# Performance work log

Hardware: AMD Instinct MI355X
Metric: run time of the kernel (lower is better)

Reference implementation:

```python
import jax, jax.numpy as jnp
import numpy as np

# SamplesLoss('sinkhorn', p=2, blur=0.05, scaling=0.5, diameter=2.0, debias=True, backend='tensorized')
P = 2
BLUR = 0.05
SCALING = 0.5
DIAMETER = 2.0


def epsilon_schedule(p, diameter, blur, scaling):
    # geomloss epsilon annealing: diameter^p -> blur^p, geometric in eps
    eps_list = (
        [diameter ** p]
        + [np.exp(e) for e in np.arange(p * np.log(diameter), p * np.log(blur), p * np.log(scaling))]
        + [blur ** p]
    )
    return [float(e) for e in eps_list]


def softmin(eps, C, h):
    # soft C-transform: f_i = -eps * log sum_j exp(h_j - C_ij/eps)
    # C: (B,N,M), h: (B,M) -> (B,N)
    return -eps * jax.scipy.special.logsumexp(h[:, None, :] - C / eps, axis=2)


def sq_cost(x, y):
    # SqDist(x,y)/2 : (B,N,D),(B,M,D) -> (B,N,M)
    x2 = jnp.sum(x * x, axis=-1)[:, :, None]
    y2 = jnp.sum(y * y, axis=-1)[:, None, :]
    return (x2 + y2 - 2.0 * jnp.einsum('bnd,bmd->bnm', x, y)) * 0.5


def setup_inputs() -> dict:
    key = jax.random.key(0)
    k1, k2 = jax.random.split(key)
    x = jax.random.uniform(k1, (8, 2048, 3), dtype=jnp.float32)
    y = jax.random.uniform(k2, (8, 2048, 3), dtype=jnp.float32)
    return {"x": x, "y": y}


def reference(x, y):
    B, N, _ = x.shape
    M = y.shape[1]
    # uniform weights (SamplesLoss default when only point clouds are given)
    a_log = jnp.full((B, N), -float(np.log(N)), dtype=x.dtype)
    b_log = jnp.full((B, M), -float(np.log(M)), dtype=y.dtype)

    C_xy = sq_cost(x, y)                 # (B,N,M)
    C_yx = jnp.swapaxes(C_xy, 1, 2)      # (B,M,N)
    C_xx = sq_cost(x, x)                 # (B,N,N) debias term
    C_yy = sq_cost(y, y)                 # (B,M,M) debias term

    eps_list = epsilon_schedule(P, DIAMETER, BLUR, SCALING)

    # initialization at the coarsest temperature (balanced OT: damping = 1)
    eps0 = eps_list[0]
    f_aa = softmin(eps0, C_xx, a_log)
    g_bb = softmin(eps0, C_yy, b_log)
    g_ab = softmin(eps0, C_yx, a_log)
    f_ba = softmin(eps0, C_xy, b_log)

    # symmetric Sinkhorn loop with epsilon scaling (no grad tracked in torch here)
    for eps in eps_list:
        ft_ba = softmin(eps, C_xy, b_log + g_ab / eps)
        gt_ab = softmin(eps, C_yx, a_log + f_ba / eps)
        f_ba = 0.5 * (f_ba + ft_ba)
        g_ab = 0.5 * (g_ab + gt_ab)
        ft_aa = softmin(eps, C_xx, a_log + f_aa / eps)
        gt_bb = softmin(eps, C_yy, b_log + g_bb / eps)
        f_aa = 0.5 * (f_aa + ft_aa)
        g_bb = 0.5 * (g_bb + gt_bb)

    # last extrapolation step, with detached dual potentials (torch .detach())
    eps = eps_list[-1]
    sg = jax.lax.stop_gradient
    f_ba, g_ab = (
        softmin(eps, C_xy, b_log + sg(g_ab) / eps),
        softmin(eps, C_yx, a_log + sg(f_ba) / eps),
    )
    f_aa = softmin(eps, C_xx, a_log + sg(f_aa) / eps)
    g_bb = softmin(eps, C_yy, b_log + sg(g_bb) / eps)

    # debiased Sinkhorn divergence, batch mode -> (B,)
    a = jnp.exp(a_log)
    b = jnp.exp(b_log)
    return jnp.sum(a * (f_ba - f_aa), axis=-1) + jnp.sum(b * (g_ab - g_bb), axis=-1)
```

## Files before the change

### kernel.cpp

```cpp
#include <hip/hip_runtime.h>
#include <math.h>

#define BATCH 8
#define NPTS 2048
#define THREADS 256
#define HALF_COLS 1024
#define NTILES_H 64
#define FRAGS 2
#define ROWS_PER_WAVE 32
#define ROWS_PER_BLOCK 128
#define LOG_M 7.62559580411076

typedef __attribute__((ext_vector_type(8))) __bf16 bf16x8;
typedef __attribute__((ext_vector_type(4))) float f32x4;

union FragU { unsigned short u[8]; uint4 v; };

__device__ __forceinline__ unsigned short f2bf(float f) {
    union { float f; unsigned u; } x; x.f = f;
    unsigned r = x.u + 0x7FFFu + ((x.u >> 16) & 1u);
    return (unsigned short)(r >> 16);
}
__device__ __forceinline__ float bf2f(unsigned short b) {
    union { unsigned u; float f; } x; x.u = ((unsigned)b) << 16;
    return x.f;
}

__global__ __launch_bounds__(THREADS) void softmin_pass(
    const float* __restrict__ x, const float* __restrict__ y,
    const float* __restrict__ potSrc, float* __restrict__ potDst,
    float sigma, float k2, float inv_k2, float rowc0, int avg)
{
    __shared__ uint4 BF[NTILES_H][32];
    __shared__ uint4 AF[4][FRAGS][32];
    __shared__ float NM[ROWS_PER_BLOCK];

    const int type  = blockIdx.z;
    const int batch = blockIdx.y;

    const float* rowP;
    const float* colP;
    int hslot, oslot;
    if (type == 0)      { rowP = x; colP = y; hslot = 1; oslot = 0; }
    else if (type == 1) { rowP = y; colP = x; hslot = 0; oslot = 1; }
    else if (type == 2) { rowP = x; colP = x; hslot = 2; oslot = 2; }
    else                { rowP = y; colP = y; hslot = 3; oslot = 3; }

    rowP += batch * NPTS * 3;
    colP += batch * NPTS * 3;
    const float* hP   = potSrc + (hslot * BATCH + batch) * NPTS;
    const float* oldP = potSrc + (oslot * BATCH + batch) * NPTS;
    float*       outP = potDst + (oslot * BATCH + batch) * NPTS;

    {
        const int t = threadIdx.x;
        const int w = t >> 6, fr = (t >> 5) & 1, idx = t & 31;
        const int row = blockIdx.x * ROWS_PER_BLOCK + w * ROWS_PER_WAVE
                      + fr * 16 + (idx & 15);
        float x0 = rowP[3 * row + 0], x1 = rowP[3 * row + 1], x2 = rowP[3 * row + 2];
        float p0 = sigma * (x0 - 0.5f), p1 = sigma * (x1 - 0.5f), p2 = sigma * (x2 - 0.5f);
        unsigned short h0 = f2bf(p0); unsigned short l0 = f2bf(p0 - bf2f(h0));
        unsigned short h1 = f2bf(p1); unsigned short l1 = f2bf(p1 - bf2f(h1));
        unsigned short h2 = f2bf(p2); unsigned short l2 = f2bf(p2 - bf2f(h2));
        FragU f;
        if (idx < 16) {
            f.u[0] = h0; f.u[1] = h0; f.u[2] = l0; f.u[3] = l0;
            f.u[4] = h1; f.u[5] = h1; f.u[6] = l1; f.u[7] = l1;
        } else {
            f.u[0] = h2; f.u[1] = h2; f.u[2] = l2; f.u[3] = l2;
            f.u[4] = 0x3F80; f.u[5] = 0x3F80; f.u[6] = 0x3F80; f.u[7] = 0;
        }
        AF[w][fr][idx] = f.v;
    }

    if (threadIdx.x < ROWS_PER_BLOCK) {
        const int i = blockIdx.x * ROWS_PER_BLOCK + threadIdx.x;
        float x0 = rowP[3 * i + 0], x1 = rowP[3 * i + 1], x2 = rowP[3 * i + 2];
        float p0 = x0 - 0.5f, p1 = x1 - 0.5f, p2 = x2 - 0.5f;
        float rowconst = 0.5f * (p0 * p0 + p1 * p1 + p2 * p2) + rowc0;
        NM[threadIdx.x] = (oldP[i] - rowconst) * inv_k2;
    }

    const int lane = threadIdx.x & 63;
    const int wave = threadIdx.x >> 6;
    const int lidx = lane & 31;
    const int quad = lane >> 4;

    float s[FRAGS][4] = {{0,0,0,0},{0,0,0,0}};
    bf16x8 af0, af1;
    f32x4 nm0, nm1;

    for (int h = 0; h < 2; ++h) {
        if (h) __syncthreads();

        for (int jj = threadIdx.x; jj < HALF_COLS; jj += THREADS) {
            const int j = h * HALF_COLS + jj;
            float y0 = colP[3 * j + 0], y1 = colP[3 * j + 1], y2 = colP[3 * j + 2];
            float p0 = y0 - 0.5f, p1 = y1 - 0.5f, p2 = y2 - 0.5f;
            unsigned short h0 = f2bf(p0); unsigned short l0 = f2bf(p0 - bf2f(h0));
            unsigned short h1 = f2bf(p1); unsigned short l1 = f2bf(p1 - bf2f(h1));
            unsigned short h2 = f2bf(p2); unsigned short l2 = f2bf(p2 - bf2f(h2));
            float hhe = sigma * (hP[j] - 0.5f * (p0 * p0 + p1 * p1 + p2 * p2));
            unsigned short hA = f2bf(hhe); float r1 = hhe - bf2f(hA);
            unsigned short hB = f2bf(r1);  float r2 = r1 - bf2f(hB);
            unsigned short hC = f2bf(r2);
            FragU f0, f1;
            f0.u[0] = h0; f0.u[1] = l0; f0.u[2] = h0; f0.u[3] = l0;
            f0.u[4] = h1; f0.u[5] = l1; f0.u[6] = h1; f0.u[7] = l1;
            f1.u[0] = h2; f1.u[1] = l2; f1.u[2] = h2; f1.u[3] = l2;
            f1.u[4] = hA; f1.u[5] = hB; f1.u[6] = hC; f1.u[7] = 0;
            BF[jj >> 4][jj & 15]        = f0.v;
            BF[jj >> 4][16 + (jj & 15)] = f1.v;
        }
        __syncthreads();

        if (h == 0) {
            af0 = *(const bf16x8*)&AF[wave][0][lidx];
            af1 = *(const bf16x8*)&AF[wave][1][lidx];
            nm0 = *(const f32x4*)&NM[wave * ROWS_PER_WAVE + quad * 4];
            nm1 = *(const f32x4*)&NM[wave * ROWS_PER_WAVE + 16 + quad * 4];
        }

        #pragma unroll 4
        for (int t = 0; t < NTILES_H; ++t) {
            bf16x8 bf = *(const bf16x8*)&BF[t][lidx];
            f32x4 a0 = __builtin_amdgcn_mfma_f32_16x16x32_bf16(af0, bf, nm0, 0, 0, 0);
            f32x4 a1 = __builtin_amdgcn_mfma_f32_16x16x32_bf16(af1, bf, nm1, 0, 0, 0);
            #pragma unroll
            for (int r = 0; r < 4; ++r) {
                s[0][r] += __builtin_amdgcn_exp2f(a0[r]);
                s[1][r] += __builtin_amdgcn_exp2f(a1[r]);
            }
        }
    }

    #pragma unroll
    for (int off = 1; off <= 8; off <<= 1)
        #pragma unroll
        for (int f = 0; f < FRAGS; ++f)
            #pragma unroll
            for (int r = 0; r < 4; ++r)
                s[f][r] += __shfl_xor(s[f][r], off, 64);

    if ((lane & 15) == 0) {
        #pragma unroll
        for (int f = 0; f < FRAGS; ++f) {
            #pragma unroll
            for (int r = 0; r < 4; ++r) {
                const int i = blockIdx.x * ROWS_PER_BLOCK + wave * ROWS_PER_WAVE
                            + f * 16 + quad * 4 + r;
                float oldv = oldP[i];
                float res = oldv - k2 * __log2f(s[f][r]);
                outP[i] = avg ? 0.5f * (oldv + res) : res;
            }
        }
    }
}

__global__ void reduce_out(const float* __restrict__ pot, float* __restrict__ out)
{
    const int batch = blockIdx.x;
    const float* fba = pot + (0 * BATCH + batch) * NPTS;
    const float* gab = pot + (1 * BATCH + batch) * NPTS;
    const float* faa = pot + (2 * BATCH + batch) * NPTS;
    const float* gbb = pot + (3 * BATCH + batch) * NPTS;

    float s = 0.0f;
    for (int i = threadIdx.x; i < NPTS; i += blockDim.x)
        s += (fba[i] - faa[i]) + (gab[i] - gbb[i]);

    #pragma unroll
    for (int off = 32; off >= 1; off >>= 1)
        s += __shfl_xor(s, off, 64);

    __shared__ float red[THREADS / 64];
    const int lane = threadIdx.x & 63;
    const int wave = threadIdx.x >> 6;
    if (lane == 0) red[wave] = s;
    __syncthreads();
    if (threadIdx.x == 0) {
        float t = 0.0f;
        for (int w = 0; w < THREADS / 64; ++w) t += red[w];
        out[batch] = t * (1.0f / NPTS);
    }
}

extern "C" void kernel_launch(void* const* d_in, const int* in_sizes, int n_in,
                              void* d_out, int out_size, void* d_ws, size_t ws_size,
                              hipStream_t stream)
{
    const float* x = (const float*)d_in[0];
    const float* y = (const float*)d_in[1];
    float* out = (float*)d_out;

    const size_t potElems = (size_t)4 * BATCH * NPTS;
    float* P0 = (float*)d_ws;
    float* P1 = P0 + potElems;

    hipMemsetAsync(P0, 0, potElems * sizeof(float), stream);

    double epsl[16];
    int ne = 0;
    epsl[ne++] = 4.0;
    const double stop = 2.0 * log(0.05);
    const double step = 2.0 * log(0.5);
    for (double e = 2.0 * log(2.0); e > stop; e += step)
        epsl[ne++] = exp(e);
    epsl[ne++] = 0.05 * 0.05;

    float* src = P0;
    float* dst = P1;
    dim3 grid(NPTS / ROWS_PER_BLOCK, BATCH, 4);

    auto launch = [&](double eps, int avg) {
        float sigma  = (float)(M_LOG2E / (2.0 * eps));
        float k2     = (float)(eps * M_LN2);
        float inv_k2 = (float)(1.0 / (eps * M_LN2));
        float rowc0  = (float)(eps * LOG_M);
        softmin_pass<<<grid, THREADS, 0, stream>>>(
            x, y, src, dst, sigma, k2, inv_k2, rowc0, avg);
        float* t = src; src = dst; dst = t;
    };

    launch(epsl[0], 0);
    for (int k = 0; k < ne; ++k)
        launch(epsl[k], 1);
    launch(epsl[ne - 1], 0);

    reduce_out<<<dim3(BATCH), THREADS, 0, stream>>>(src, out);
}
```

Before: 284.6 us.

## Switch to 32x32x16 MFMA tiles with column-split waves and LDS row reduction

Replaces the 16x16x32 bf16 MFMA (two fragments per wave, 128 rows per block) with the 32x32x16 variant. Each pair of waves shares 32 rows and splits the column tiles, and partial row sums are merged through shared memory before the log step. Blocks shrink to 64 rows, doubling the grid, and sigma's scaling is adjusted to match the new operand packing. The intent is higher MFMA throughput per instruction and more blocks for occupancy, at the cost of an extra LDS reduction and barrier. Each MFMA now feeds 16 exp2 calls, so exp throughput probably remains the bottleneck.

```diff
diff --git a/kernel.cpp b/kernel.cpp
--- a/kernel.cpp
+++ b/kernel.cpp
@@ -5,14 +5,12 @@
 #define NPTS 2048
 #define THREADS 256
 #define HALF_COLS 1024
-#define NTILES_H 64
-#define FRAGS 2
-#define ROWS_PER_WAVE 32
-#define ROWS_PER_BLOCK 128
+#define TILES_H 32
+#define ROWS_PER_BLOCK 64
 #define LOG_M 7.62559580411076
 
-typedef __attribute__((ext_vector_type(8))) __bf16 bf16x8;
-typedef __attribute__((ext_vector_type(4))) float f32x4;
+typedef __attribute__((ext_vector_type(8)))  __bf16 bf16x8;
+typedef __attribute__((ext_vector_type(16))) float  f32x16;
 
 union FragU { unsigned short u[8]; uint4 v; };
 
@@ -31,9 +29,10 @@
     const float* __restrict__ potSrc, float* __restrict__ potDst,
     float sigma, float k2, float inv_k2, float rowc0, int avg)
 {
-    __shared__ uint4 BF[NTILES_H][32];
-    __shared__ uint4 AF[4][FRAGS][32];
+    __shared__ uint4 BF[TILES_H][64];
+    __shared__ uint4 AF[2][64];
     __shared__ float NM[ROWS_PER_BLOCK];
+    __shared__ float SRED[2][2][32];
 
     const int type  = blockIdx.z;
     const int batch = blockIdx.y;
@@ -52,43 +51,43 @@
     const float* oldP = potSrc + (oslot * BATCH + batch) * NPTS;
     float*       outP = potDst + (oslot * BATCH + batch) * NPTS;
 
-    {
-        const int t = threadIdx.x;
-        const int w = t >> 6, fr = (t >> 5) & 1, idx = t & 31;
-        const int row = blockIdx.x * ROWS_PER_BLOCK + w * ROWS_PER_WAVE
-                      + fr * 16 + (idx & 15);
+    if (threadIdx.x < 128) {
+        const int g = threadIdx.x >> 6, idx = threadIdx.x & 63;
+        const int row = blockIdx.x * ROWS_PER_BLOCK + g * 32 + (idx & 31);
         float x0 = rowP[3 * row + 0], x1 = rowP[3 * row + 1], x2 = rowP[3 * row + 2];
         float p0 = sigma * (x0 - 0.5f), p1 = sigma * (x1 - 0.5f), p2 = sigma * (x2 - 0.5f);
         unsigned short h0 = f2bf(p0); unsigned short l0 = f2bf(p0 - bf2f(h0));
         unsigned short h1 = f2bf(p1); unsigned short l1 = f2bf(p1 - bf2f(h1));
         unsigned short h2 = f2bf(p2); unsigned short l2 = f2bf(p2 - bf2f(h2));
         FragU f;
-        if (idx < 16) {
+        if (idx < 32) {
             f.u[0] = h0; f.u[1] = h0; f.u[2] = l0; f.u[3] = l0;
             f.u[4] = h1; f.u[5] = h1; f.u[6] = l1; f.u[7] = l1;
         } else {
             f.u[0] = h2; f.u[1] = h2; f.u[2] = l2; f.u[3] = l2;
             f.u[4] = 0x3F80; f.u[5] = 0x3F80; f.u[6] = 0x3F80; f.u[7] = 0;
         }
-        AF[w][fr][idx] = f.v;
-    }
-
-    if (threadIdx.x < ROWS_PER_BLOCK) {
-        const int i = blockIdx.x * ROWS_PER_BLOCK + threadIdx.x;
+        AF[g][idx] = f.v;
+    } else if (threadIdx.x < 128 + ROWS_PER_BLOCK) {
+        const int r = threadIdx.x - 128;
+        const int i = blockIdx.x * ROWS_PER_BLOCK + r;
         float x0 = rowP[3 * i + 0], x1 = rowP[3 * i + 1], x2 = rowP[3 * i + 2];
         float p0 = x0 - 0.5f, p1 = x1 - 0.5f, p2 = x2 - 0.5f;
         float rowconst = 0.5f * (p0 * p0 + p1 * p1 + p2 * p2) + rowc0;
-        NM[threadIdx.x] = (oldP[i] - rowconst) * inv_k2;
+        NM[r] = (oldP[i] - rowconst) * inv_k2;
     }
 
     const int lane = threadIdx.x & 63;
     const int wave = threadIdx.x >> 6;
-    const int lidx = lane & 31;
-    const int quad = lane >> 4;
-
-    float s[FRAGS][4] = {{0,0,0,0},{0,0,0,0}};
-    bf16x8 af0, af1;
-    f32x4 nm0, nm1;
+    const int g    = wave >> 1;
+    const int c    = wave & 1;
+    const int khalf = lane >> 5;
+
+    float s[16];
+    #pragma unroll
+    for (int r = 0; r < 16; ++r) s[r] = 0.0f;
+    bf16x8 af;
+    f32x16 nmv;
 
     for (int h = 0; h < 2; ++h) {
         if (h) __syncthreads();
@@ -109,51 +108,53 @@
             f0.u[4] = h1; f0.u[5] = l1; f0.u[6] = h1; f0.u[7] = l1;
             f1.u[0] = h2; f1.u[1] = l2; f1.u[2] = h2; f1.u[3] = l2;
             f1.u[4] = hA; f1.u[5] = hB; f1.u[6] = hC; f1.u[7] = 0;
-            BF[jj >> 4][jj & 15]        = f0.v;
-            BF[jj >> 4][16 + (jj & 15)] = f1.v;
+            BF[jj >> 5][jj & 31]        = f0.v;
+            BF[jj >> 5][32 + (jj & 31)] = f1.v;
         }
         __syncthreads();
 
         if (h == 0) {
-            af0 = *(const bf16x8*)&AF[wave][0][lidx];
-            af1 = *(const bf16x8*)&AF[wave][1][lidx];
-            nm0 = *(const f32x4*)&NM[wave * ROWS_PER_WAVE + quad * 4];
-            nm1 = *(const f32x4*)&NM[wave * ROWS_PER_WAVE + 16 + quad * 4];
-        }
-
-        #pragma unroll 4
-        for (int t = 0; t < NTILES_H; ++t) {
-            bf16x8 bf = *(const bf16x8*)&BF[t][lidx];
-            f32x4 a0 = __builtin_amdgcn_mfma_f32_16x16x32_bf16(af0, bf, nm0, 0, 0, 0);
-            f32x4 a1 = __builtin_amdgcn_mfma_f32_16x16x32_bf16(af1, bf, nm1, 0, 0, 0);
+            af = *(const bf16x8*)&AF[g][lane];
             #pragma unroll
-            for (int r = 0; r < 4; ++r) {
-                s[0][r] += __builtin_amdgcn_exp2f(a0[r]);
-                s[1][r] += __builtin_amdgcn_exp2f(a1[r]);
+            for (int r = 0; r < 16; ++r) {
+                const int row = (r & 3) + 8 * (r >> 2) + 4 * khalf;
+                nmv[r] = NM[g * 32 + row];
             }
         }
+
+        const int tbase = c * (TILES_H / 2);
+        #pragma unroll 2
+        for (int t = 0; t < TILES_H / 2; ++t) {
+            bf16x8 bf = *(const bf16x8*)&BF[tbase + t][lane];
+            f32x16 acc = __builtin_amdgcn_mfma_f32_32x32x16_bf16(af, bf, nmv, 0, 0, 0);
+            #pragma unroll
+            for (int r = 0; r < 16; ++r)
+                s[r] += __builtin_amdgcn_exp2f(acc[r]);
+        }
     }
 
     #pragma unroll
-    for (int off = 1; off <= 8; off <<= 1)
+    for (int off = 1; off <= 16; off <<= 1)
         #pragma unroll
-        for (int f = 0; f < FRAGS; ++f)
-            #pragma unroll
-            for (int r = 0; r < 4; ++r)
-                s[f][r] += __shfl_xor(s[f][r], off, 64);
-
-    if ((lane & 15) == 0) {
+        for (int r = 0; r < 16; ++r)
+            s[r] += __shfl_xor(s[r], off, 64);
+
+    if ((lane & 31) == 0) {
         #pragma unroll
-        for (int f = 0; f < FRAGS; ++f) {
-            #pragma unroll
-            for (int r = 0; r < 4; ++r) {
-                const int i = blockIdx.x * ROWS_PER_BLOCK + wave * ROWS_PER_WAVE
-                            + f * 16 + quad * 4 + r;
-                float oldv = oldP[i];
-                float res = oldv - k2 * __log2f(s[f][r]);
-                outP[i] = avg ? 0.5f * (oldv + res) : res;
-            }
-        }
+        for (int r = 0; r < 16; ++r) {
+            const int row = (r & 3) + 8 * (r >> 2) + 4 * khalf;
+            SRED[g][c][row] = s[r];
+        }
+    }
+    __syncthreads();
+
+    if (threadIdx.x < ROWS_PER_BLOCK) {
+        const int p = threadIdx.x >> 5, r = threadIdx.x & 31;
+        const int i = blockIdx.x * ROWS_PER_BLOCK + p * 32 + r;
+        float sum = SRED[p][0][r] + SRED[p][1][r];
+        float oldv = oldP[i];
+        float res = oldv - k2 * __log2f(sum);
+        outP[i] = avg ? 0.5f * (oldv + res) : res;
     }
 }
 
@@ -213,7 +214,7 @@
     dim3 grid(NPTS / ROWS_PER_BLOCK, BATCH, 4);
 
     auto launch = [&](double eps, int avg) {
-        float sigma  = (float)(M_LOG2E / (2.0 * eps));
+        float sigma  = (float)(M_LOG2E / eps);
         float k2     = (float)(eps * M_LN2);
         float inv_k2 = (float)(1.0 / (eps * M_LN2));
         float rowc0  = (float)(eps * LOG_M);
```

Result: faster. 268.1 us (-5.8%).
